# Optimization experiments

Hardware: AMD Instinct MI355X
Metric: run time of the kernel (lower is better)

## Reference

```python
import jax, jax.numpy as jnp
from jax import lax
import numpy as np

B, T = 2, 4096
NQ, NAUX, NR, NS, K = 256, 28, 512, 256, 2
DIL = [2 ** i for i in range(10)] * 3  # 30 residual blocks
L = len(DIL)


def _causal_conv(x, w, b, d):
    # x: (B, Cin, T), w: (Cout, Cin, K) -- left-pad (K-1)*d for causality
    pad = (w.shape[-1] - 1) * d
    y = lax.conv_general_dilated(x, w, window_strides=(1,), padding=[(pad, 0)],
                                 rhs_dilation=(d,),
                                 dimension_numbers=('NCH', 'OIH', 'NCH'))
    return y + b[None, :, None]


def _conv1x1(x, w, b):
    # x: (B, Cin, T), w: (Cout, Cin)
    return jnp.einsum('oc,bct->bot', w, x) + b[None, :, None]


def setup_inputs() -> dict:
    key = jax.random.key(0)
    ks = jax.random.split(key, 32)
    s = 0.05
    n = lambda k, shp: (jax.random.normal(k, shp, dtype=jnp.float32) * s)
    return {
        'x': jax.random.randint(ks[0], (B, T), 0, NQ, dtype=jnp.int32),
        'h': jax.random.normal(ks[1], (B, NAUX, T), dtype=jnp.float32),
        'causal_w': n(ks[2], (NR, NQ, K)), 'causal_b': n(ks[3], (NR,)),
        'dil_sig_w': n(ks[4], (L, NR, NR, K)), 'dil_sig_b': n(ks[5], (L, NR)),
        'dil_tanh_w': n(ks[6], (L, NR, NR, K)), 'dil_tanh_b': n(ks[7], (L, NR)),
        'aux_sig_w': n(ks[8], (L, NR, NAUX)), 'aux_sig_b': n(ks[9], (L, NR)),
        'aux_tanh_w': n(ks[10], (L, NR, NAUX)), 'aux_tanh_b': n(ks[11], (L, NR)),
        'skip_w': n(ks[12], (L, NS, NR)), 'skip_b': n(ks[13], (L, NS)),
        'res_w': n(ks[14], (L, NR, NR)), 'res_b': n(ks[15], (L, NR)),
        'post1_w': n(ks[16], (NS, NS)), 'post1_b': n(ks[17], (NS,)),
        'post2_w': n(ks[18], (NQ, NS)), 'post2_b': n(ks[19], (NQ,)),
        'lin_w': n(ks[20], (NQ, NQ)), 'lin_b': n(ks[21], (NQ,)),
    }


def reference(x, h, causal_w, causal_b, dil_sig_w, dil_sig_b, dil_tanh_w,
              dil_tanh_b, aux_sig_w, aux_sig_b, aux_tanh_w, aux_tanh_b,
              skip_w, skip_b, res_w, res_b, post1_w, post1_b, post2_w,
              post2_b, lin_w, lin_b):
    # preprocess: one-hot -> (B, NQ, T) -> causal conv
    oh = jax.nn.one_hot(x % NQ, NQ, dtype=jnp.float32).transpose(0, 2, 1)
    out = _causal_conv(oh, causal_w, causal_b, 1)  # (B, NR, T)
    skip_sum = jnp.zeros((B, NS, T), dtype=jnp.float32)
    for l, d in enumerate(DIL):
        s = _causal_conv(out, dil_sig_w[l], dil_sig_b[l], d) \
            + _conv1x1(h, aux_sig_w[l], aux_sig_b[l])
        t = _causal_conv(out, dil_tanh_w[l], dil_tanh_b[l], d) \
            + _conv1x1(h, aux_tanh_w[l], aux_tanh_b[l])
        g = jax.nn.sigmoid(s) * jnp.tanh(t)  # gated activation (B, NR, T)
        skip_sum = skip_sum + _conv1x1(g, skip_w[l], skip_b[l])
        out = _conv1x1(g, res_w[l], res_b[l]) + out  # residual
    o = jax.nn.relu(skip_sum)
    o = jax.nn.relu(_conv1x1(o, post1_w, post1_b))
    o = _conv1x1(o, post2_w, post2_b).transpose(0, 2, 1)  # (B, T, NQ)
    return o @ lin_w.T + lin_b
```

## Files before the change

### kernel.cpp

```cpp
#include <hip/hip_runtime.h>
#include <cstddef>

#define B_ 2
#define T_ 4096
#define NQ_ 256
#define NAUX_ 28
#define NR_ 512
#define NS_ 256
#define L_ 30

typedef _Float16 half_t;
typedef __attribute__((ext_vector_type(8))) _Float16 f16x8;
typedef __attribute__((ext_vector_type(4))) _Float16 f16x4;
typedef __attribute__((ext_vector_type(4))) float f32x4;

__device__ inline half_t f2h(float f) { return (half_t)f; }
__device__ inline float h2f(half_t h) { return (float)h; }

__device__ __forceinline__ void gload16(const void* g, void* l) {
    __builtin_amdgcn_global_load_lds(
        (const __attribute__((address_space(1))) unsigned int*)g,
        (__attribute__((address_space(3))) unsigned int*)l, 16, 0, 0);
}


__global__ __launch_bounds__(256, 2) void gates_gemm(
    const half_t* __restrict__ actB, const half_t* __restrict__ Wf,
    const float* __restrict__ biasG, half_t* __restrict__ g,
    const half_t* __restrict__ zbuf, int dil)
{
    __shared__ __align__(16) half_t sB[2][128 * 64];

    const int tid = threadIdx.x;
    const int b = blockIdx.z;
    const int tB = blockIdx.x * 128;
    const int w = tid >> 6, lane = tid & 63;
    const int wm = w >> 1, wn = w & 1;
    const int l15 = lane & 15, lg = lane >> 4;
    const int rr = lane >> 3, cc = lane & 7;
    const int sc8 = cc ^ rr;

    f32x4 acc[4][4] = {};
    f16x8 a0[8], a1[8];

    const int mgW = blockIdx.y * 8 + wm * 4;

    auto loadA = [&](f16x8* d, int kc) {
#pragma unroll
        for (int i = 0; i < 4; i++)
#pragma unroll
            for (int s = 0; s < 2; s++)
                d[i * 2 + s] = *(const f16x8*)&Wf[((size_t)(mgW + i) * 34 + kc * 2 + s) * 512 + lane * 8];
    };
    auto stageB = [&](int kc, int buf) {
#pragma unroll
        for (int it = 0; it < 4; it++) {
            const int t = tB + w * 32 + it * 8 + rr;
            const half_t* p;
            if (kc < 8) {
                p = actB + ((size_t)b * T_ + t) * 576 + kc * 64;
            } else if (kc < 16) {
                const int tp = t - dil;
                p = (tp >= 0) ? actB + ((size_t)b * T_ + tp) * 576 + (kc - 8) * 64
                              : zbuf;
            } else {
                p = actB + ((size_t)b * T_ + t) * 576 + 512;
            }
            gload16(p + sc8 * 8, &sB[buf][(w * 32 + it * 8) * 64]);
        }
    };
    auto compute = [&](const f16x8* a, int buf) {
#pragma unroll
        for (int s = 0; s < 2; s++) {
            f16x8 bv[4];
#pragma unroll
            for (int j = 0; j < 4; j++) {
                const int r = wn * 64 + j * 16 + l15;
                bv[j] = *(const f16x8*)&sB[buf][r * 64 + (((s * 4 + lg) ^ (l15 & 7)) * 8)];
            }
#pragma unroll
            for (int i = 0; i < 4; i++)
#pragma unroll
                for (int j = 0; j < 4; j++)
                    acc[i][j] = __builtin_amdgcn_mfma_f32_16x16x32_f16(a[i * 2 + s], bv[j], acc[i][j], 0, 0, 0);
        }
    };

    stageB(0, 0);
    loadA(a0, 0);
#pragma unroll
    for (int kc = 0; kc < 17; kc++) {
        __syncthreads();
        if (kc + 1 < 17) {
            stageB(kc + 1, (kc + 1) & 1);
            loadA((kc & 1) ? a0 : a1, kc + 1);
        }
        compute((kc & 1) ? a1 : a0, kc & 1);
    }

    const int gidx = blockIdx.y * 2 + wm;
    const int t0 = tB + wn * 64 + l15;
#pragma unroll
    for (int i = 0; i < 2; i++) {
        const int c = gidx * 32 + i * 16 + lg * 4;
        const float4 bs = *(const float4*)&biasG[gidx * 64 + i * 16 + lg * 4];
        const float4 bt4 = *(const float4*)&biasG[gidx * 64 + 32 + i * 16 + lg * 4];
        const float bsa[4] = {bs.x, bs.y, bs.z, bs.w};
        const float bta[4] = {bt4.x, bt4.y, bt4.z, bt4.w};
#pragma unroll
        for (int j = 0; j < 4; j++) {
            const int t = t0 + j * 16;
            f16x4 o;
#pragma unroll
            for (int e = 0; e < 4; e++) {
                const float sv = acc[i][j][e] + bsa[e];
                const float tv = acc[i + 2][j][e] + bta[e];
                const float sg = 1.f / (1.f + __expf(-sv));
                const float ex = __expf(-2.f * tv);
                const float th = (1.f - ex) / (1.f + ex);
                o[e] = f2h(sg * th);
            }
            *(f16x4*)(g + ((size_t)b * T_ + t) * 512 + c) = o;
        }
    }
}

template<int K, int EPI>
__global__ __launch_bounds__(256, 2) void gemm_mfma(
    const half_t* __restrict__ X, const half_t* __restrict__ Wf,
    const float* __restrict__ bias, void* __restrict__ out, int M,
    half_t* __restrict__ actB, half_t* __restrict__ skipH)
{
    constexpr int NK = K / 64;
    constexpr int NKS = K / 32;
    __shared__ __align__(16) half_t sB[2][128 * 64];

    const int tid = threadIdx.x;
    const int b = blockIdx.z;
    const int tB = blockIdx.x * 128;
    const int mB = blockIdx.y * 128;
    const int w = tid >> 6, lane = tid & 63;
    const int wm = w >> 1, wn = w & 1;
    const int l15 = lane & 15, lg = lane >> 4;
    const int rr = lane >> 3, cc = lane & 7;
    const int sc8 = cc ^ rr;

    f32x4 acc[4][4] = {};
    f16x8 a0[8], a1[8];

    const int mgW = (mB >> 4) + wm * 4;
    const half_t* Xb = X + ((size_t)b * T_ + tB) * K;

    auto loadA = [&](f16x8* d, int kc) {
#pragma unroll
        for (int i = 0; i < 4; i++)
#pragma unroll
            for (int s = 0; s < 2; s++)
                d[i * 2 + s] = *(const f16x8*)&Wf[((size_t)(mgW + i) * NKS + kc * 2 + s) * 512 + lane * 8];
    };
    auto stageB = [&](int kc, int buf) {
#pragma unroll
        for (int it = 0; it < 4; it++) {
            const int row = w * 32 + it * 8;
            gload16(Xb + (size_t)(row + rr) * K + kc * 64 + sc8 * 8,
                    &sB[buf][row * 64]);
        }
    };
    auto compute = [&](const f16x8* a, int buf) {
#pragma unroll
        for (int s = 0; s < 2; s++) {
            f16x8 bv[4];
#pragma unroll
            for (int j = 0; j < 4; j++) {
                const int r = wn * 64 + j * 16 + l15;
                bv[j] = *(const f16x8*)&sB[buf][r * 64 + (((s * 4 + lg) ^ (l15 & 7)) * 8)];
            }
#pragma unroll
            for (int i = 0; i < 4; i++)
#pragma unroll
                for (int j = 0; j < 4; j++)
                    acc[i][j] = __builtin_amdgcn_mfma_f32_16x16x32_f16(a[i * 2 + s], bv[j], acc[i][j], 0, 0, 0);
        }
    };

    stageB(0, 0);
    loadA(a0, 0);
#pragma unroll
    for (int kc = 0; kc < NK; kc++) {
        __syncthreads();
        if (kc + 1 < NK) {
            stageB(kc + 1, (kc + 1) & 1);
            loadA((kc & 1) ? a0 : a1, kc + 1);
        }
        compute((kc & 1) ? a1 : a0, kc & 1);
    }

    const int n0 = tB + wn * 64 + l15;
#pragma unroll
    for (int i = 0; i < 4; i++) {
        const int m = mB + wm * 64 + i * 16 + lg * 4;
        float4 bv = make_float4(0.f, 0.f, 0.f, 0.f);
        if (bias) bv = *(const float4*)&bias[m];
#pragma unroll
        for (int j = 0; j < 4; j++) {
            const int t = n0 + j * 16;
            float o0 = acc[i][j][0] + bv.x, o1 = acc[i][j][1] + bv.y;
            float o2 = acc[i][j][2] + bv.z, o3 = acc[i][j][3] + bv.w;
            if (EPI == 1) {
                o0 = fmaxf(o0, 0.f); o1 = fmaxf(o1, 0.f);
                o2 = fmaxf(o2, 0.f); o3 = fmaxf(o3, 0.f);
            }
            if (EPI == 3) {
                const size_t bt = (size_t)b * T_ + t;
                half_t* p = (mB < 512) ? (actB + bt * 576 + m)
                                       : (skipH + bt * 256 + (m - 512));
                f16x4 old = *(const f16x4*)p;
                f16x4 nv = {f2h(h2f(old.x) + o0), f2h(h2f(old.y) + o1),
                            f2h(h2f(old.z) + o2), f2h(h2f(old.w) + o3)};
                *(f16x4*)p = nv;
            } else {
                const size_t off = ((size_t)b * T_ + t) * M + m;
                if (EPI == 2) {
                    *(float4*)((float*)out + off) = make_float4(o0, o1, o2, o3);
                } else {
                    f16x4 ov = {f2h(o0), f2h(o1), f2h(o2), f2h(o3)};
                    *(f16x4*)((half_t*)out + off) = ov;
                }
            }
        }
    }
}

__global__ __launch_bounds__(256) void relupack_kernel(
    const half_t* __restrict__ skipH, half_t* __restrict__ outp)
{
    const int idx = blockIdx.x * 256 + threadIdx.x;
    const int c = (idx & 63) * 4;
    const int bt = idx >> 6;
    const f16x4 v = *(const f16x4*)(skipH + (size_t)bt * 256 + c);
    f16x4 o = {f2h(fmaxf(h2f(v.x), 0.f)), f2h(fmaxf(h2f(v.y), 0.f)),
               f2h(fmaxf(h2f(v.z), 0.f)), f2h(fmaxf(h2f(v.w), 0.f))};
    *(f16x4*)(outp + (size_t)bt * 256 + c) = o;
}

__global__ __launch_bounds__(256) void embed_kernel(
    const int* __restrict__ x, const float* __restrict__ cw,
    const float* __restrict__ cb, half_t* __restrict__ actB)
{
    const int t = blockIdx.x, b = blockIdx.y;
    const int idc = x[b * T_ + t];
    const int idp = (t > 0) ? x[b * T_ + t - 1] : -1;
    const size_t bt = (size_t)b * T_ + t;
    for (int c = threadIdx.x; c < 512; c += 256) {
        float v = cw[(c * 256 + idc) * 2 + 1] + cb[c];
        if (idp >= 0) v += cw[(c * 256 + idp) * 2 + 0];
        actB[bt * 576 + c] = f2h(v);
    }
}

__global__ __launch_bounds__(256) void packh_kernel(
    const float* __restrict__ h, half_t* __restrict__ actB)
{
    const int idx = blockIdx.x * 256 + threadIdx.x;
    const int j = idx & 63;
    const int bt = idx >> 6;
    const int b = bt >> 12, t = bt & 4095;
    const float v = (j < 28) ? h[((size_t)b * NAUX_ + j) * T_ + t] : 0.f;
    actB[(size_t)bt * 576 + 512 + j] = f2h(v);
}

__global__ __launch_bounds__(256) void packgate_kernel(
    const float* __restrict__ dsw, const float* __restrict__ dtw,
    half_t* __restrict__ Wg)
{
    const int idx = blockIdx.x * 256 + threadIdx.x;
    const int lane = idx & 63;
    const int ks = (idx >> 6) & 15;
    const int mg = (idx >> 10) & 63;
    const int l = idx >> 16;
    const int r = mg * 16 + (lane & 15);
    const int rsub = r & 63;
    const int c = (r >> 6) * 32 + (rsub & 31);
    const float* src = (rsub < 32) ? dsw : dtw;
    const size_t base = ((size_t)(l * 512 + c) * 512 + ks * 32 + (lane >> 4) * 8) * 2;
    const float4* p = (const float4*)(src + base);
    const float4 q0 = p[0], q1 = p[1], q2 = p[2], q3 = p[3];
    f16x8 cur = {f2h(q0.y), f2h(q0.w), f2h(q1.y), f2h(q1.w),
                 f2h(q2.y), f2h(q2.w), f2h(q3.y), f2h(q3.w)};
    f16x8 pst = {f2h(q0.x), f2h(q0.z), f2h(q1.x), f2h(q1.z),
                 f2h(q2.x), f2h(q2.z), f2h(q3.x), f2h(q3.z)};
    half_t* dst = Wg + (size_t)l * 1114112;
    *(f16x8*)&dst[((size_t)(mg * 34 + ks) * 64 + lane) * 8] = cur;
    *(f16x8*)&dst[((size_t)(mg * 34 + 16 + ks) * 64 + lane) * 8] = pst;
}

__global__ __launch_bounds__(256) void packgaux_kernel(
    const float* __restrict__ asw, const float* __restrict__ atw,
    half_t* __restrict__ Wg)
{
    const int idx = blockIdx.x * 256 + threadIdx.x;
    const int lane = idx & 63;
    const int ksd = (idx >> 6) & 1;
    const int mg = (idx >> 7) & 63;
    const int l = idx >> 13;
    const int r = mg * 16 + (lane & 15);
    const int rsub = r & 63;
    const int c = (r >> 6) * 32 + (rsub & 31);
    const float* src = (rsub < 32) ? asw : atw;
    const int j0 = ksd * 32 + (lane >> 4) * 8;
    f16x8 v = {};
#pragma unroll
    for (int e = 0; e < 8; e++) {
        const int j = j0 + e;
        if (j < NAUX_) v[e] = f2h(src[(size_t)(l * 512 + c) * NAUX_ + j]);
    }
    Wg += (size_t)l * 1114112;
    *(f16x8*)&Wg[((size_t)(mg * 34 + 32 + ksd) * 64 + lane) * 8] = v;
}

__global__ __launch_bounds__(256) void packsr_kernel(
    const float* __restrict__ rsw, const float* __restrict__ skw,
    half_t* __restrict__ Wsr)
{
    const int idx = blockIdx.x * 256 + threadIdx.x;
    const int lane = idx & 63;
    const int ks = (idx >> 6) & 15;
    const int mg = (idx >> 10) % 48;
    const int l = (idx >> 10) / 48;
    const int r = mg * 16 + (lane & 15);
    const int kb = ks * 32 + (lane >> 4) * 8;
    const float* src = (r < 512) ? (rsw + ((size_t)l * 512 + r) * 512 + kb)
                                 : (skw + ((size_t)l * 256 + (r - 512)) * 512 + kb);
    const float4 q0 = ((const float4*)src)[0], q1 = ((const float4*)src)[1];
    f16x8 v = {f2h(q0.x), f2h(q0.y), f2h(q0.z), f2h(q0.w),
               f2h(q1.x), f2h(q1.y), f2h(q1.z), f2h(q1.w)};
    *(f16x8*)&Wsr[(size_t)l * 393216 + ((size_t)(mg * 16 + ks) * 64 + lane) * 8] = v;
}

__global__ __launch_bounds__(256) void packpost_kernel(
    const float* __restrict__ p1w, const float* __restrict__ p2w,
    const float* __restrict__ lw, half_t* __restrict__ Wpost)
{
    const int idx = blockIdx.x * 256 + threadIdx.x;
    const int lane = idx & 63;
    const int ks = (idx >> 6) & 7;
    const int mg = (idx >> 9) & 15;
    const int mi = idx >> 13;
    const float* src = (mi == 0) ? p1w : (mi == 1) ? p2w : lw;
    const int r = mg * 16 + (lane & 15);
    const int kb = ks * 32 + (lane >> 4) * 8;
    const float4 q0 = ((const float4*)(src + (size_t)r * 256 + kb))[0];
    const float4 q1 = ((const float4*)(src + (size_t)r * 256 + kb))[1];
    f16x8 v = {f2h(q0.x), f2h(q0.y), f2h(q0.z), f2h(q0.w),
               f2h(q1.x), f2h(q1.y), f2h(q1.z), f2h(q1.w)};
    *(f16x8*)&Wpost[(size_t)mi * 65536 + ((size_t)(mg * 8 + ks) * 64 + lane) * 8] = v;
}

__global__ __launch_bounds__(256) void packbias_kernel(
    const float* __restrict__ dsb, const float* __restrict__ asb,
    const float* __restrict__ dtb, const float* __restrict__ atb,
    const float* __restrict__ rsb, const float* __restrict__ skb,
    float* __restrict__ biasG, float* __restrict__ biasSr)
{
    const int idx = blockIdx.x * 256 + threadIdx.x;
    if (idx < 30 * 1024) {
        const int l = idx >> 10, r = idx & 1023;
        const int rsub = r & 63;
        const int c = (r >> 6) * 32 + (rsub & 31);
        const float v = (rsub < 32) ? (dsb[l * 512 + c] + asb[l * 512 + c])
                                    : (dtb[l * 512 + c] + atb[l * 512 + c]);
        biasG[idx] = v;
    } else if (idx < 30 * 1024 + 30 * 768) {
        const int j = idx - 30 * 1024;
        const int l = j / 768, r = j % 768;
        biasSr[j] = (r < 512) ? rsb[l * 512 + r] : skb[l * 256 + (r - 512)];
    }
}

extern "C" void kernel_launch(void* const* d_in, const int* in_sizes, int n_in,
                              void* d_out, int out_size, void* d_ws, size_t ws_size,
                              hipStream_t stream)
{
    (void)in_sizes; (void)n_in; (void)out_size; (void)ws_size;

    const int* x = (const int*)d_in[0];
    const float* h = (const float*)d_in[1];
    const float* causal_w = (const float*)d_in[2];
    const float* causal_b = (const float*)d_in[3];
    const float* dsw = (const float*)d_in[4];
    const float* dsb = (const float*)d_in[5];
    const float* dtw = (const float*)d_in[6];
    const float* dtb = (const float*)d_in[7];
    const float* asw = (const float*)d_in[8];
    const float* asb = (const float*)d_in[9];
    const float* atw = (const float*)d_in[10];
    const float* atb = (const float*)d_in[11];
    const float* skw = (const float*)d_in[12];
    const float* skb = (const float*)d_in[13];
    const float* rsw = (const float*)d_in[14];
    const float* rsb = (const float*)d_in[15];
    const float* p1w = (const float*)d_in[16];
    const float* p1b = (const float*)d_in[17];
    const float* p2w = (const float*)d_in[18];
    const float* p2b = (const float*)d_in[19];
    const float* lw  = (const float*)d_in[20];
    const float* lb  = (const float*)d_in[21];

    char* ws = (char*)d_ws;
    size_t off = 0;
    auto alloc = [&](size_t bytes) { char* p = ws + off; off += (bytes + 255) & ~(size_t)255; return p; };

    half_t* Wg     = (half_t*)alloc((size_t)L_ * 1114112 * 2);
    half_t* Wsr    = (half_t*)alloc((size_t)L_ * 393216 * 2);
    half_t* Wpost  = (half_t*)alloc((size_t)3 * 65536 * 2);
    float*  biasG  = (float*) alloc((size_t)L_ * 1024 * 4);
    float*  biasSr = (float*) alloc((size_t)L_ * 768 * 4);
    half_t* actB   = (half_t*)alloc((size_t)B_ * T_ * 576 * 2);
    half_t* g      = (half_t*)alloc((size_t)B_ * T_ * 512 * 2);
    half_t* skipH  = (half_t*)alloc((size_t)B_ * T_ * 256 * 2);
    half_t* zbuf   = (half_t*)alloc(256);
    half_t* pA     = (half_t*)alloc((size_t)B_ * T_ * 256 * 2);
    half_t* pB     = (half_t*)alloc((size_t)B_ * T_ * 256 * 2);

    hipMemsetAsync(skipH, 0, (size_t)B_ * T_ * 256 * 2 + 256, stream);

    packgate_kernel<<<30 * 64 * 16 * 64 / 256, 256, 0, stream>>>(dsw, dtw, Wg);
    packgaux_kernel<<<30 * 64 * 2 * 64 / 256, 256, 0, stream>>>(asw, atw, Wg);
    packsr_kernel<<<30 * 48 * 16 * 64 / 256, 256, 0, stream>>>(rsw, skw, Wsr);
    packpost_kernel<<<3 * 16 * 8 * 64 / 256, 256, 0, stream>>>(p1w, p2w, lw, Wpost);
    packbias_kernel<<<(30 * 1024 + 30 * 768 + 255) / 256, 256, 0, stream>>>(
        dsb, asb, dtb, atb, rsb, skb, biasG, biasSr);
    packh_kernel<<<B_ * T_ * 64 / 256, 256, 0, stream>>>(h, actB);
    embed_kernel<<<dim3(T_, B_), 256, 0, stream>>>(x, causal_w, causal_b, actB);

    for (int l = 0; l < L_; l++) {
        const int dil = 1 << (l % 10);
        gates_gemm<<<dim3(32, 8, B_), 256, 0, stream>>>(
            actB, Wg + (size_t)l * 1114112, biasG + (size_t)l * 1024, g, zbuf, dil);
        gemm_mfma<512, 3><<<dim3(32, 6, B_), 256, 0, stream>>>(
            g, Wsr + (size_t)l * 393216, biasSr + (size_t)l * 768, nullptr, 768,
            actB, skipH);
    }

    relupack_kernel<<<B_ * T_ * 64 / 256, 256, 0, stream>>>(skipH, pA);
    gemm_mfma<256, 1><<<dim3(32, 2, B_), 256, 0, stream>>>(pA, Wpost, p1b, pB, 256,
                                                           nullptr, nullptr);
    gemm_mfma<256, 0><<<dim3(32, 2, B_), 256, 0, stream>>>(pB, Wpost + 65536, p2b, pA, 256,
                                                           nullptr, nullptr);
    gemm_mfma<256, 2><<<dim3(32, 2, B_), 256, 0, stream>>>(pA, Wpost + 131072, lb, d_out, 256,
                                                           nullptr, nullptr);
}
```

Before: 1.535 ms.

## Stage two K-slices per barrier in gates and 1x1 GEMM kernels

Doubles the LDS tile so each pipeline step stages two 64-wide K slices, which halves the number of __syncthreads barriers per GEMM. In the gates kernel the current-tap and dilated-tap slices are paired in each step. Weight register loads are interleaved between the two compute halves so they overlap MFMA work. LDS use grows to 64 KB per block, which may limit occupancy at two blocks per CU.

```diff
diff --git a/kernel.cpp b/kernel.cpp
--- a/kernel.cpp
+++ b/kernel.cpp
@@ -29,7 +29,7 @@
     const float* __restrict__ biasG, half_t* __restrict__ g,
     const half_t* __restrict__ zbuf, int dil)
 {
-    __shared__ __align__(16) half_t sB[2][128 * 64];
+    __shared__ __align__(16) half_t sB[2][256 * 64];
 
     const int tid = threadIdx.x;
     const int b = blockIdx.z;
@@ -41,41 +41,41 @@
     const int sc8 = cc ^ rr;
 
     f32x4 acc[4][4] = {};
-    f16x8 a0[8], a1[8];
+    f16x8 aC[8], aP[8];
 
     const int mgW = blockIdx.y * 8 + wm * 4;
 
-    auto loadA = [&](f16x8* d, int kc) {
+    auto loadA = [&](f16x8* d, int v) {
 #pragma unroll
         for (int i = 0; i < 4; i++)
 #pragma unroll
             for (int s = 0; s < 2; s++)
-                d[i * 2 + s] = *(const f16x8*)&Wf[((size_t)(mgW + i) * 34 + kc * 2 + s) * 512 + lane * 8];
-    };
-    auto stageB = [&](int kc, int buf) {
+                d[i * 2 + s] = *(const f16x8*)&Wf[((size_t)(mgW + i) * 34 + v * 2 + s) * 512 + lane * 8];
+    };
+    auto stageSlice = [&](int v, int rowbase, int buf) {
 #pragma unroll
         for (int it = 0; it < 4; it++) {
             const int t = tB + w * 32 + it * 8 + rr;
             const half_t* p;
-            if (kc < 8) {
-                p = actB + ((size_t)b * T_ + t) * 576 + kc * 64;
-            } else if (kc < 16) {
+            if (v < 8) {
+                p = actB + ((size_t)b * T_ + t) * 576 + v * 64;
+            } else if (v < 16) {
                 const int tp = t - dil;
-                p = (tp >= 0) ? actB + ((size_t)b * T_ + tp) * 576 + (kc - 8) * 64
+                p = (tp >= 0) ? actB + ((size_t)b * T_ + tp) * 576 + (v - 8) * 64
                               : zbuf;
             } else {
                 p = actB + ((size_t)b * T_ + t) * 576 + 512;
             }
-            gload16(p + sc8 * 8, &sB[buf][(w * 32 + it * 8) * 64]);
-        }
-    };
-    auto compute = [&](const f16x8* a, int buf) {
+            gload16(p + sc8 * 8, &sB[buf][(rowbase + w * 32 + it * 8) * 64]);
+        }
+    };
+    auto compute = [&](const f16x8* a, int rowbase, int buf) {
 #pragma unroll
         for (int s = 0; s < 2; s++) {
             f16x8 bv[4];
 #pragma unroll
             for (int j = 0; j < 4; j++) {
-                const int r = wn * 64 + j * 16 + l15;
+                const int r = rowbase + wn * 64 + j * 16 + l15;
                 bv[j] = *(const f16x8*)&sB[buf][r * 64 + (((s * 4 + lg) ^ (l15 & 7)) * 8)];
             }
 #pragma unroll
@@ -86,16 +86,28 @@
         }
     };
 
-    stageB(0, 0);
-    loadA(a0, 0);
-#pragma unroll
-    for (int kc = 0; kc < 17; kc++) {
+    stageSlice(0, 0, 0);
+    stageSlice(8, 128, 0);
+    loadA(aC, 0);
+    loadA(aP, 8);
+#pragma unroll
+    for (int kc = 0; kc < 9; kc++) {
         __syncthreads();
-        if (kc + 1 < 17) {
-            stageB(kc + 1, (kc + 1) & 1);
-            loadA((kc & 1) ? a0 : a1, kc + 1);
-        }
-        compute((kc & 1) ? a1 : a0, kc & 1);
+        const int nb = (kc + 1) & 1;
+        if (kc < 7) {
+            stageSlice(kc + 1, 0, nb);
+            stageSlice(kc + 9, 128, nb);
+        } else if (kc == 7) {
+            stageSlice(16, 0, nb);
+        }
+        if (kc < 8) {
+            compute(aC, 0, kc & 1);
+            loadA(aC, (kc < 7) ? (kc + 1) : 16);
+            compute(aP, 128, kc & 1);
+            if (kc < 7) loadA(aP, kc + 9);
+        } else {
+            compute(aC, 0, kc & 1);
+        }
     }
 
     const int gidx = blockIdx.y * 2 + wm;
@@ -131,9 +143,9 @@
     const float* __restrict__ bias, void* __restrict__ out, int M,
     half_t* __restrict__ actB, half_t* __restrict__ skipH)
 {
-    constexpr int NK = K / 64;
+    constexpr int NITER = K / 128;
     constexpr int NKS = K / 32;
-    __shared__ __align__(16) half_t sB[2][128 * 64];
+    __shared__ __align__(16) half_t sB[2][256 * 64];
 
     const int tid = threadIdx.x;
     const int b = blockIdx.z;
@@ -146,33 +158,33 @@
     const int sc8 = cc ^ rr;
 
     f32x4 acc[4][4] = {};
-    f16x8 a0[8], a1[8];
+    f16x8 aC[8], aP[8];
 
     const int mgW = (mB >> 4) + wm * 4;
     const half_t* Xb = X + ((size_t)b * T_ + tB) * K;
 
-    auto loadA = [&](f16x8* d, int kc) {
+    auto loadA = [&](f16x8* d, int v) {
 #pragma unroll
         for (int i = 0; i < 4; i++)
 #pragma unroll
             for (int s = 0; s < 2; s++)
-                d[i * 2 + s] = *(const f16x8*)&Wf[((size_t)(mgW + i) * NKS + kc * 2 + s) * 512 + lane * 8];
-    };
-    auto stageB = [&](int kc, int buf) {
+                d[i * 2 + s] = *(const f16x8*)&Wf[((size_t)(mgW + i) * NKS + v * 2 + s) * 512 + lane * 8];
+    };
+    auto stageSlice = [&](int v, int rowbase, int buf) {
 #pragma unroll
         for (int it = 0; it < 4; it++) {
             const int row = w * 32 + it * 8;
-            gload16(Xb + (size_t)(row + rr) * K + kc * 64 + sc8 * 8,
-                    &sB[buf][row * 64]);
-        }
-    };
-    auto compute = [&](const f16x8* a, int buf) {
+            gload16(Xb + (size_t)(row + rr) * K + v * 64 + sc8 * 8,
+                    &sB[buf][(rowbase + row) * 64]);
+        }
+    };
+    auto compute = [&](const f16x8* a, int rowbase, int buf) {
 #pragma unroll
         for (int s = 0; s < 2; s++) {
             f16x8 bv[4];
 #pragma unroll
             for (int j = 0; j < 4; j++) {
-                const int r = wn * 64 + j * 16 + l15;
+                const int r = rowbase + wn * 64 + j * 16 + l15;
                 bv[j] = *(const f16x8*)&sB[buf][r * 64 + (((s * 4 + lg) ^ (l15 & 7)) * 8)];
             }
 #pragma unroll
@@ -183,16 +195,21 @@
         }
     };
 
-    stageB(0, 0);
-    loadA(a0, 0);
-#pragma unroll
-    for (int kc = 0; kc < NK; kc++) {
+    stageSlice(0, 0, 0);
+    stageSlice(1, 128, 0);
+    loadA(aC, 0);
+    loadA(aP, 1);
+#pragma unroll
+    for (int kc = 0; kc < NITER; kc++) {
         __syncthreads();
-        if (kc + 1 < NK) {
-            stageB(kc + 1, (kc + 1) & 1);
-            loadA((kc & 1) ? a0 : a1, kc + 1);
-        }
-        compute((kc & 1) ? a1 : a0, kc & 1);
+        if (kc + 1 < NITER) {
+            stageSlice(2 * kc + 2, 0, (kc + 1) & 1);
+            stageSlice(2 * kc + 3, 128, (kc + 1) & 1);
+        }
+        compute(aC, 0, kc & 1);
+        if (kc + 1 < NITER) loadA(aC, 2 * kc + 2);
+        compute(aP, 128, kc & 1);
+        if (kc + 1 < NITER) loadA(aP, 2 * kc + 3);
     }
 
     const int n0 = tB + wn * 64 + l15;
```

After: 1.516 ms. No clear change (-1.2%).
